# Optimization experiments

Measured on AMD Instinct MI355X. Metric: run time of the kernel, lower is better.

## Reference

```python
import jax, jax.numpy as jnp
import numpy as np

N_NODES = 100000
N_EDGES = 1600000
F_IN, HID, N_CLS = 512, 256, 40


def setup_inputs() -> dict:
    key = jax.random.key(0)
    k1, k2, k3, k4 = jax.random.split(key, 4)
    features = jax.random.normal(k1, (N_NODES, F_IN), dtype=jnp.float32)
    # Glorot-ish scaled weights
    W1 = jax.random.normal(k2, (F_IN, HID), dtype=jnp.float32) * (1.0 / np.sqrt(F_IN))
    b1 = jnp.zeros((HID,), dtype=jnp.float32)
    W2 = jax.random.normal(k3, (HID, N_CLS), dtype=jnp.float32) * (1.0 / np.sqrt(HID))
    b2 = jnp.zeros((N_CLS,), dtype=jnp.float32)
    edge_index = jax.random.randint(k4, (2, N_EDGES), 0, N_NODES, dtype=jnp.int64)
    return {"features": features, "W1": W1, "b1": b1, "W2": W2, "b2": b2,
            "edge_index": edge_index}


def _gcn_conv(x, W, b, src, dst, n_nodes):
    # PyG GCNConv: h = X W; out = D^{-1/2}(A+I)D^{-1/2} h + b
    h = x @ W  # [N, out]
    # degree with self-loops (in-degree on dst + 1)
    deg = jax.ops.segment_sum(jnp.ones_like(dst, dtype=h.dtype), dst,
                              num_segments=n_nodes) + 1.0
    dinv = jax.lax.rsqrt(deg)  # [N]
    norm = dinv[src] * dinv[dst]  # [E]
    # gather-normalize-scatter over edges, plus self-loop term dinv_i^2 * h_i
    agg = jax.ops.segment_sum(h[src] * norm[:, None], dst, num_segments=n_nodes)
    agg = agg + h * (dinv * dinv)[:, None]
    return agg + b


def reference(features, W1, b1, W2, b2, edge_index):
    src, dst = edge_index[0], edge_index[1]
    n = features.shape[0]
    x = jax.nn.relu(_gcn_conv(features, W1, b1, src, dst, n))
    # dropout is identity in eval mode (training=False)
    x = _gcn_conv(x, W2, b2, src, dst, n)
    return jax.nn.log_softmax(x, axis=1), jax.nn.softmax(x, axis=1)
```

## Files before the change

### kernel.cpp

```cpp
#include <hip/hip_runtime.h>
#include <hip/hip_bf16.h>


#define F_IN 512
#define HID  256
#define NCLS 40
#define NPAD 48

typedef __attribute__((ext_vector_type(8))) short bf16x8;
typedef __attribute__((ext_vector_type(4))) float floatx4;

__device__ inline unsigned short f2bf(float v) {
    unsigned u = __float_as_uint(v);
    u += 0x7fffu + ((u >> 16) & 1u);
    return (unsigned short)(u >> 16);
}
__device__ inline float bf2f(unsigned short u) {
    return __uint_as_float(((unsigned)u) << 16);
}

__device__ inline void gload_lds16(const void* g, void* l) {
    __builtin_amdgcn_global_load_lds(
        (const __attribute__((address_space(1))) unsigned int*)g,
        (__attribute__((address_space(3))) unsigned int*)l, 16, 0, 0);
}

__device__ inline bf16x8 pack8(float4 f0, float4 f1) {
    bf16x8 r;
    r[0] = (short)f2bf(f0.x); r[1] = (short)f2bf(f0.y);
    r[2] = (short)f2bf(f0.z); r[3] = (short)f2bf(f0.w);
    r[4] = (short)f2bf(f1.x); r[5] = (short)f2bf(f1.y);
    r[6] = (short)f2bf(f1.z); r[7] = (short)f2bf(f1.w);
    return r;
}

__global__ void detect64_kernel(const int* __restrict__ ei, int* __restrict__ flag) {
    __shared__ int any_nz;
    if (threadIdx.x == 0) any_nz = 0;
    __syncthreads();
    int nz = 0;
    for (int i = threadIdx.x; i < 4096; i += 256) {
        nz |= (ei[2 * i + 1] != 0);
    }
    if (nz) atomicOr(&any_nz, 1);
    __syncthreads();
    if (threadIdx.x == 0) *flag = any_nz ? 0 : 1;
}

__device__ inline int edge_src(const int* ei, long long E, int e, int is64) {
    return is64 ? ei[2LL * e] : ei[e];
}
__device__ inline int edge_dst(const int* ei, long long E, int e, int is64) {
    return is64 ? ei[2LL * (E + e)] : ei[(int)E + e];
}

__global__ void count_kernel(const int* __restrict__ ei, int E,
                             const int* __restrict__ flag, int* __restrict__ cnt) {
    int e = blockIdx.x * 256 + threadIdx.x;
    if (e >= E) return;
    int is64 = *flag;
    int d = edge_dst(ei, E, e, is64);
    atomicAdd(&cnt[d], 1);
}

__global__ __launch_bounds__(256) void scan_block_sums(const int* __restrict__ cnt,
                                                       int* __restrict__ blockSums, int Nn) {
    __shared__ int sdata[256];
    int b = blockIdx.x, t = threadIdx.x;
    int sum = 0;
    int i0 = b * 1024 + t * 4;
    for (int i = 0; i < 4; ++i) {
        int idx = i0 + i;
        if (idx < Nn) sum += cnt[idx];
    }
    sdata[t] = sum;
    __syncthreads();
    for (int s = 128; s > 0; s >>= 1) {
        if (t < s) sdata[t] += sdata[t + s];
        __syncthreads();
    }
    if (t == 0) blockSums[b] = sdata[0];
}

__global__ void scan_sums_kernel(int* __restrict__ blockSums, int nB,
                                 int* __restrict__ rowStart, int Nn) {
    if (threadIdx.x == 0 && blockIdx.x == 0) {
        int run = 0;
        for (int i = 0; i < nB; ++i) { int v = blockSums[i]; blockSums[i] = run; run += v; }
        rowStart[Nn] = run;
    }
}

__global__ __launch_bounds__(256) void scan_final(const int* __restrict__ cnt,
                                                  const int* __restrict__ blockSumsEx,
                                                  int* __restrict__ rowStart,
                                                  int* __restrict__ rowPos, int Nn) {
    __shared__ int sdata[256];
    int b = blockIdx.x, t = threadIdx.x;
    int base = blockSumsEx[b];
    int vals[4];
    int sum = 0;
    int i0 = b * 1024 + t * 4;
    for (int i = 0; i < 4; ++i) {
        int idx = i0 + i;
        vals[i] = (idx < Nn) ? cnt[idx] : 0;
        sum += vals[i];
    }
    sdata[t] = sum;
    __syncthreads();
    for (int off = 1; off < 256; off <<= 1) {
        int y = (t >= off) ? sdata[t - off] : 0;
        __syncthreads();
        sdata[t] += y;
        __syncthreads();
    }
    int run = base + (sdata[t] - sum);
    for (int i = 0; i < 4; ++i) {
        int idx = i0 + i;
        if (idx < Nn) { rowStart[idx] = run; rowPos[idx] = run; }
        run += vals[i];
    }
}

__global__ void dinv_kernel(const int* __restrict__ cnt, float* __restrict__ dinv, int Nn) {
    int i = blockIdx.x * 256 + threadIdx.x;
    if (i < Nn) dinv[i] = rsqrtf((float)cnt[i] + 1.0f);
}

__global__ void fill_kernel(const int* __restrict__ ei, int E, const int* __restrict__ flag,
                            const float* __restrict__ dinv, int* __restrict__ rowPos,
                            int* __restrict__ csrSrc, float* __restrict__ csrNorm) {
    int e = blockIdx.x * 256 + threadIdx.x;
    if (e >= E) return;
    int is64 = *flag;
    int s = edge_src(ei, E, e, is64);
    int d = edge_dst(ei, E, e, is64);
    int p = atomicAdd(&rowPos[d], 1);
    csrSrc[p] = s;
    csrNorm[p] = dinv[s] * dinv[d];
}

__global__ __launch_bounds__(256) void convertW1t_kernel(const float* __restrict__ W1,
                                                         unsigned short* __restrict__ W1t) {
    int id = blockIdx.x * 256 + threadIdx.x;
    int k = id >> 8, n = id & 255;
    W1t[n * 512 + k] = f2bf(W1[id]);
}

__global__ __launch_bounds__(256) void convertW2t_kernel(const float* __restrict__ W2,
                                                         unsigned short* __restrict__ W2t) {
    int id = blockIdx.x * 256 + threadIdx.x;
    if (id >= NPAD * HID) return;
    int n = id / HID, k = id % HID;
    W2t[id] = (n < NCLS) ? f2bf(W2[k * NCLS + n]) : (unsigned short)0;
}

#define BK 64
__global__ __launch_bounds__(256) void gemm1_mfma_kernel(const float* __restrict__ X,
                                                         const unsigned short* __restrict__ W1t,
                                                         unsigned short* __restrict__ h1, int Nn) {
    __shared__ float As[128 * 64];
    __shared__ unsigned short Bs[128 * 64];
    const int tid = threadIdx.x;
    const int bm = blockIdx.x * 128;
    const int bn = blockIdx.y * 128;
    const int lane = tid & 63, w = tid >> 6;
    const int wr = (w & 1) * 64, wc = (w >> 1) * 64;
    const int lrow = lane & 15, lq = lane >> 4;

    int aRow[8], aK[8], bRow[4], bK[4];
#pragma unroll
    for (int i = 0; i < 8; ++i) {
        int c = i * 256 + w * 64 + lane;
        int row = c >> 4, pslot = c & 15;
        aRow[i] = row; aK[i] = (pslot ^ (row & 15)) * 4;
    }
#pragma unroll
    for (int i = 0; i < 4; ++i) {
        int c = i * 256 + w * 64 + lane;
        int row = c >> 3, pslot = c & 7;
        bRow[i] = row; bK[i] = (pslot ^ (row & 7)) * 8;
    }

    floatx4 acc[4][4];
#pragma unroll
    for (int i = 0; i < 4; ++i)
#pragma unroll
        for (int j = 0; j < 4; ++j)
            acc[i][j] = (floatx4){0.f, 0.f, 0.f, 0.f};

    for (int t = 0; t < F_IN / BK; ++t) {
        const int k0 = t * BK;
        __syncthreads();
#pragma unroll
        for (int i = 0; i < 8; ++i) {
            int srow = bm + aRow[i];
            if (srow >= Nn) srow = Nn - 1;
            gload_lds16(&X[(size_t)srow * F_IN + k0 + aK[i]],
                        &As[(i * 256 + w * 64) * 4]);
        }
#pragma unroll
        for (int i = 0; i < 4; ++i)
            gload_lds16(&W1t[(size_t)(bn + bRow[i]) * F_IN + k0 + bK[i]],
                        &Bs[(i * 256 + w * 64) * 8]);
        __syncthreads();

#pragma unroll
        for (int kh = 0; kh < 2; ++kh) {
            bf16x8 av[4], bv[4];
#pragma unroll
            for (int mt = 0; mt < 4; ++mt) {
                int row = wr + mt * 16 + lrow;
                int m = row & 15;
                int s0 = kh * 8 + lq * 2;
                float4 f0 = *(const float4*)&As[row * 64 + ((s0 ^ m) << 2)];
                float4 f1 = *(const float4*)&As[row * 64 + (((s0 + 1) ^ m) << 2)];
                av[mt] = pack8(f0, f1);
            }
#pragma unroll
            for (int nt = 0; nt < 4; ++nt) {
                int row = wc + nt * 16 + lrow;
                int ls = kh * 4 + lq;
                bv[nt] = *(const bf16x8*)&Bs[row * 64 + ((ls ^ (row & 7)) << 3)];
            }
#pragma unroll
            for (int mt = 0; mt < 4; ++mt)
#pragma unroll
                for (int nt = 0; nt < 4; ++nt)
                    acc[mt][nt] = __builtin_amdgcn_mfma_f32_16x16x32_bf16(
                        bv[nt], av[mt], acc[mt][nt], 0, 0, 0);
        }
    }

#pragma unroll
    for (int mt = 0; mt < 4; ++mt) {
        size_t gm = (size_t)(bm + wr + mt * 16 + lrow);
#pragma unroll
        for (int nt = 0; nt < 4; ++nt) {
            int gn = bn + wc + nt * 16 + lq * 4;
            ushort4 o;
            o.x = f2bf(acc[mt][nt][0]); o.y = f2bf(acc[mt][nt][1]);
            o.z = f2bf(acc[mt][nt][2]); o.w = f2bf(acc[mt][nt][3]);
            *(ushort4*)&h1[gm * HID + gn] = o;
        }
    }
}

__global__ __launch_bounds__(256) void agg1_kernel(const unsigned short* __restrict__ h1,
                                                   const int* __restrict__ rowStart,
                                                   const int* __restrict__ csrSrc,
                                                   const float* __restrict__ csrNorm,
                                                   const float* __restrict__ dinv,
                                                   const float* __restrict__ b1,
                                                   unsigned short* __restrict__ x1b, int Nn) {
    int n = blockIdx.x * 4 + (threadIdx.x >> 6);
    int lane = threadIdx.x & 63;
    if (n >= Nn) return;
    const int half = lane >> 5;
    const int col = lane & 31;
    const char* hb = (const char*)h1 + col * 16;

    float acc[8];
#pragma unroll
    for (int j = 0; j < 8; ++j) acc[j] = 0.f;

    int s0 = rowStart[n], s1 = rowStart[n + 1];
    int e = s0;
    for (; e + 7 < s1; e += 8) {
#pragma unroll
        for (int p = 0; p < 4; ++p) {
            int idx = csrSrc[e + 2 * p + half];
            float nrm = csrNorm[e + 2 * p + half];
            bf16x8 v = *(const bf16x8*)(hb + (unsigned)idx * (unsigned)(HID * 2));
#pragma unroll
            for (int j = 0; j < 8; ++j)
                acc[j] += nrm * bf2f((unsigned short)v[j]);
        }
    }
    for (; e + 1 < s1; e += 2) {
        int idx = csrSrc[e + half];
        float nrm = csrNorm[e + half];
        bf16x8 v = *(const bf16x8*)(hb + (unsigned)idx * (unsigned)(HID * 2));
#pragma unroll
        for (int j = 0; j < 8; ++j)
            acc[j] += nrm * bf2f((unsigned short)v[j]);
    }
    if (e < s1) {
        int idx = csrSrc[e];
        float nrm = half ? 0.f : csrNorm[e];
        bf16x8 v = *(const bf16x8*)(hb + (unsigned)idx * (unsigned)(HID * 2));
#pragma unroll
        for (int j = 0; j < 8; ++j)
            acc[j] += nrm * bf2f((unsigned short)v[j]);
    }

#pragma unroll
    for (int j = 0; j < 8; ++j) acc[j] += __shfl_xor(acc[j], 32);

    if (half == 0) {
        float di = dinv[n];
        float self = di * di;
        bf16x8 hv = *(const bf16x8*)(hb + (unsigned)n * (unsigned)(HID * 2));
        float4 bv0 = *(const float4*)(b1 + col * 8);
        float4 bv1 = *(const float4*)(b1 + col * 8 + 4);
        float bb[8] = {bv0.x, bv0.y, bv0.z, bv0.w, bv1.x, bv1.y, bv1.z, bv1.w};
        bf16x8 o;
#pragma unroll
        for (int j = 0; j < 8; ++j)
            o[j] = (short)f2bf(fmaxf(acc[j] + self * bf2f((unsigned short)hv[j]) + bb[j], 0.f));
        *(bf16x8*)((char*)x1b + (size_t)n * (HID * 2) + col * 16) = o;
    }
}

__global__ __launch_bounds__(256) void gemm2_mfma_kernel(const unsigned short* __restrict__ x1b,
                                                         const unsigned short* __restrict__ W2t,
                                                         unsigned short* __restrict__ h2b) {
    const int tid = threadIdx.x;
    const int lane = tid & 63, w = tid >> 6;
    const int base = blockIdx.x * 128 + w * 32;
    const int lrow = lane & 15, lq = lane >> 4;

    floatx4 acc[2][3];
#pragma unroll
    for (int i = 0; i < 2; ++i)
#pragma unroll
        for (int j = 0; j < 3; ++j)
            acc[i][j] = (floatx4){0.f, 0.f, 0.f, 0.f};

#pragma unroll
    for (int k0 = 0; k0 < HID; k0 += 32) {
        bf16x8 a[2], b[3];
#pragma unroll
        for (int mt = 0; mt < 2; ++mt)
            a[mt] = *(const bf16x8*)&x1b[(size_t)(base + mt * 16 + lrow) * HID + k0 + lq * 8];
#pragma unroll
        for (int nt = 0; nt < 3; ++nt)
            b[nt] = *(const bf16x8*)&W2t[(size_t)(nt * 16 + lrow) * HID + k0 + lq * 8];
#pragma unroll
        for (int mt = 0; mt < 2; ++mt)
#pragma unroll
            for (int nt = 0; nt < 3; ++nt)
                acc[mt][nt] = __builtin_amdgcn_mfma_f32_16x16x32_bf16(
                    b[nt], a[mt], acc[mt][nt], 0, 0, 0);
    }
#pragma unroll
    for (int mt = 0; mt < 2; ++mt) {
        size_t gm = (size_t)(base + mt * 16 + lrow);
#pragma unroll
        for (int nt = 0; nt < 3; ++nt) {
            int gn = nt * 16 + lq * 4;
            ushort4 o;
            o.x = f2bf(acc[mt][nt][0]); o.y = f2bf(acc[mt][nt][1]);
            o.z = f2bf(acc[mt][nt][2]); o.w = f2bf(acc[mt][nt][3]);
            *(ushort4*)&h2b[gm * NPAD + gn] = o;
        }
    }
}

__global__ __launch_bounds__(256) void agg2_kernel(const unsigned short* __restrict__ h2b,
                                                   const int* __restrict__ rowStart,
                                                   const int* __restrict__ csrSrc,
                                                   const float* __restrict__ csrNorm,
                                                   const float* __restrict__ dinv,
                                                   const float* __restrict__ b2,
                                                   float* __restrict__ out, int Nn) {
    int n = blockIdx.x * 4 + (threadIdx.x >> 6);
    int lane = threadIdx.x & 63;
    if (n >= Nn) return;
    bool act = lane < NCLS;
    int cl = act ? lane : 0;
    float acc = 0.f;
    int s0 = rowStart[n], s1 = rowStart[n + 1];
    int e = s0;
    for (; e + 3 < s1; e += 4) {
        int iA = csrSrc[e], iB = csrSrc[e + 1], iC = csrSrc[e + 2], iD = csrSrc[e + 3];
        float nA = csrNorm[e], nB = csrNorm[e + 1], nC = csrNorm[e + 2], nD = csrNorm[e + 3];
        float vA = bf2f(h2b[(size_t)iA * NPAD + cl]);
        float vB = bf2f(h2b[(size_t)iB * NPAD + cl]);
        float vC = bf2f(h2b[(size_t)iC * NPAD + cl]);
        float vD = bf2f(h2b[(size_t)iD * NPAD + cl]);
        acc += nA * vA + nB * vB + nC * vC + nD * vD;
    }
    for (; e < s1; ++e) {
        int s = csrSrc[e];
        acc += csrNorm[e] * bf2f(h2b[(size_t)s * NPAD + cl]);
    }
    float di = dinv[n];
    acc += di * di * bf2f(h2b[(size_t)n * NPAD + cl]) + b2[cl];
    float v = act ? acc : -3.4e38f;
#pragma unroll
    for (int off = 32; off > 0; off >>= 1) v = fmaxf(v, __shfl_xor(v, off));
    float ex = act ? expf(acc - v) : 0.f;
    float ssum = ex;
#pragma unroll
    for (int off = 32; off > 0; off >>= 1) ssum += __shfl_xor(ssum, off);
    if (act) {
        float ls = acc - v - logf(ssum);
        out[(size_t)n * NCLS + lane] = ls;
        out[(size_t)Nn * NCLS + (size_t)n * NCLS + lane] = ex / ssum;
    }
}

extern "C" void kernel_launch(void* const* d_in, const int* in_sizes, int n_in,
                              void* d_out, int out_size, void* d_ws, size_t ws_size,
                              hipStream_t stream) {
    const float* features = (const float*)d_in[0];
    const float* W1 = (const float*)d_in[1];
    const float* b1 = (const float*)d_in[2];
    const float* W2 = (const float*)d_in[3];
    const float* b2 = (const float*)d_in[4];
    const int* edge_index = (const int*)d_in[5];

    const int N = in_sizes[0] / F_IN;
    const int E = in_sizes[5] / 2;
    const int Mpad = (N + 127) & ~127;
    float* out = (float*)d_out;

    auto align256 = [](size_t x) { return (x + 255) & ~(size_t)255; };
    char* w = (char*)d_ws;
    int* cnt        = (int*)w;  w += align256((size_t)N * 4);
    int* rowStart   = (int*)w;  w += align256((size_t)(N + 1) * 4);
    int* rowPos     = (int*)w;  w += align256((size_t)N * 4);
    int* blockSums  = (int*)w;  w += align256(1024 * 4);
    int* flag64     = (int*)w;  w += 256;
    int* csrSrc     = (int*)w;  w += align256((size_t)E * 4);
    float* csrNorm  = (float*)w; w += align256((size_t)E * 4);
    float* dinv     = (float*)w; w += align256((size_t)N * 4);
    unsigned short* W1t = (unsigned short*)w; w += align256((size_t)HID * F_IN * 2);
    unsigned short* W2t = (unsigned short*)w; w += align256((size_t)NPAD * HID * 2);
    unsigned short* h1  = (unsigned short*)w; w += align256((size_t)Mpad * HID * 2);
    unsigned short* x1b = (unsigned short*)w; w += align256((size_t)Mpad * HID * 2);
    unsigned short* h2b = (unsigned short*)w; w += align256((size_t)Mpad * NPAD * 2);
    (void)ws_size;

    const int nB = (N + 1023) / 1024;
    const int eBlocks = (E + 255) / 256;
    const int nBlocks = (N + 255) / 256;
    const int waveBlocks = (N + 3) / 4;

    hipMemsetAsync(cnt, 0, (size_t)N * 4, stream);
    detect64_kernel<<<1, 256, 0, stream>>>(edge_index, flag64);
    count_kernel<<<eBlocks, 256, 0, stream>>>(edge_index, E, flag64, cnt);
    scan_block_sums<<<nB, 256, 0, stream>>>(cnt, blockSums, N);
    scan_sums_kernel<<<1, 64, 0, stream>>>(blockSums, nB, rowStart, N);
    dinv_kernel<<<nBlocks, 256, 0, stream>>>(cnt, dinv, N);
    scan_final<<<nB, 256, 0, stream>>>(cnt, blockSums, rowStart, rowPos, N);
    fill_kernel<<<eBlocks, 256, 0, stream>>>(edge_index, E, flag64, dinv, rowPos,
                                             csrSrc, csrNorm);

    convertW1t_kernel<<<(F_IN * HID) / 256, 256, 0, stream>>>(W1, W1t);
    convertW2t_kernel<<<(NPAD * HID + 255) / 256, 256, 0, stream>>>(W2, W2t);

    dim3 g1(Mpad / 128, HID / 128);
    gemm1_mfma_kernel<<<g1, 256, 0, stream>>>(features, W1t, h1, N);
    agg1_kernel<<<waveBlocks, 256, 0, stream>>>(h1, rowStart, csrSrc, csrNorm, dinv,
                                                b1, x1b, N);
    gemm2_mfma_kernel<<<Mpad / 128, 256, 0, stream>>>(x1b, W2t, h2b);
    agg2_kernel<<<waveBlocks, 256, 0, stream>>>(h2b, rowStart, csrSrc, csrNorm, dinv,
                                                b2, out, N);
}
```

Before: 741.3 us.

## Split layer-1 aggregation into column slices with 16-edge lanes per wave

The layer-1 aggregation kernel now splits the 256 hidden columns into 8 slices of 32 handled by separate blocks, grid-striding over nodes. Each wave covers 16 edges in parallel with 4 lanes per edge instead of 2 edges with 32 lanes. The aim is to keep gathered rows in cache per slice and expose more memory-level parallelism for low-degree nodes. In exchange, each gather is only 64 bytes, index and norm loads are repeated for every slice, and a 4-step shuffle reduction is needed per node.

```diff
diff --git a/kernel.cpp b/kernel.cpp
--- a/kernel.cpp
+++ b/kernel.cpp
@@ -246,6 +246,7 @@
     }
 }
 
+#define AGG1_K 3200
 __global__ __launch_bounds__(256) void agg1_kernel(const unsigned short* __restrict__ h1,
                                                    const int* __restrict__ rowStart,
                                                    const int* __restrict__ csrSrc,
@@ -253,62 +254,47 @@
                                                    const float* __restrict__ dinv,
                                                    const float* __restrict__ b1,
                                                    unsigned short* __restrict__ x1b, int Nn) {
-    int n = blockIdx.x * 4 + (threadIdx.x >> 6);
-    int lane = threadIdx.x & 63;
-    if (n >= Nn) return;
-    const int half = lane >> 5;
-    const int col = lane & 31;
-    const char* hb = (const char*)h1 + col * 16;
-
-    float acc[8];
-#pragma unroll
-    for (int j = 0; j < 8; ++j) acc[j] = 0.f;
-
-    int s0 = rowStart[n], s1 = rowStart[n + 1];
-    int e = s0;
-    for (; e + 7 < s1; e += 8) {
-#pragma unroll
-        for (int p = 0; p < 4; ++p) {
-            int idx = csrSrc[e + 2 * p + half];
-            float nrm = csrNorm[e + 2 * p + half];
-            bf16x8 v = *(const bf16x8*)(hb + (unsigned)idx * (unsigned)(HID * 2));
+    const int slice = blockIdx.x & 7;
+    const int bb = blockIdx.x >> 3;
+    const int wid = threadIdx.x >> 6;
+    const int lane = threadIdx.x & 63;
+    const int eg = lane >> 2;
+    const int lc = lane & 3;
+    const char* hb = (const char*)h1 + slice * 64 + lc * 16;
+
+    const int c0 = slice * 32 + lc * 8;
+    float bia[8];
+#pragma unroll
+    for (int j = 0; j < 8; ++j) bia[j] = b1[c0 + j];
+
+    for (int n = bb * 4 + wid; n < Nn; n += AGG1_K * 4) {
+        float acc[8];
+#pragma unroll
+        for (int j = 0; j < 8; ++j) acc[j] = 0.f;
+        int s0 = rowStart[n], s1 = rowStart[n + 1];
+        for (int e = s0; e + eg < s1; e += 16) {
+            int idx = csrSrc[e + eg];
+            float nrm = csrNorm[e + eg];
+            bf16x8 v = *(const bf16x8*)(hb + (size_t)idx * (HID * 2));
 #pragma unroll
             for (int j = 0; j < 8; ++j)
                 acc[j] += nrm * bf2f((unsigned short)v[j]);
         }
-    }
-    for (; e + 1 < s1; e += 2) {
-        int idx = csrSrc[e + half];
-        float nrm = csrNorm[e + half];
-        bf16x8 v = *(const bf16x8*)(hb + (unsigned)idx * (unsigned)(HID * 2));
-#pragma unroll
-        for (int j = 0; j < 8; ++j)
-            acc[j] += nrm * bf2f((unsigned short)v[j]);
-    }
-    if (e < s1) {
-        int idx = csrSrc[e];
-        float nrm = half ? 0.f : csrNorm[e];
-        bf16x8 v = *(const bf16x8*)(hb + (unsigned)idx * (unsigned)(HID * 2));
-#pragma unroll
-        for (int j = 0; j < 8; ++j)
-            acc[j] += nrm * bf2f((unsigned short)v[j]);
-    }
-
-#pragma unroll
-    for (int j = 0; j < 8; ++j) acc[j] += __shfl_xor(acc[j], 32);
-
-    if (half == 0) {
-        float di = dinv[n];
-        float self = di * di;
-        bf16x8 hv = *(const bf16x8*)(hb + (unsigned)n * (unsigned)(HID * 2));
-        float4 bv0 = *(const float4*)(b1 + col * 8);
-        float4 bv1 = *(const float4*)(b1 + col * 8 + 4);
-        float bb[8] = {bv0.x, bv0.y, bv0.z, bv0.w, bv1.x, bv1.y, bv1.z, bv1.w};
-        bf16x8 o;
-#pragma unroll
-        for (int j = 0; j < 8; ++j)
-            o[j] = (short)f2bf(fmaxf(acc[j] + self * bf2f((unsigned short)hv[j]) + bb[j], 0.f));
-        *(bf16x8*)((char*)x1b + (size_t)n * (HID * 2) + col * 16) = o;
+#pragma unroll
+        for (int off = 4; off < 64; off <<= 1)
+#pragma unroll
+            for (int j = 0; j < 8; ++j) acc[j] += __shfl_xor(acc[j], off);
+
+        if (eg == 0) {
+            float di = dinv[n];
+            float self = di * di;
+            bf16x8 hv = *(const bf16x8*)(hb + (size_t)n * (HID * 2));
+            bf16x8 o;
+#pragma unroll
+            for (int j = 0; j < 8; ++j)
+                o[j] = (short)f2bf(fmaxf(acc[j] + self * bf2f((unsigned short)hv[j]) + bia[j], 0.f));
+            *(bf16x8*)((char*)x1b + (size_t)n * (HID * 2) + slice * 64 + lc * 16) = o;
+        }
     }
 }
 
@@ -453,7 +439,7 @@
 
     dim3 g1(Mpad / 128, HID / 128);
     gemm1_mfma_kernel<<<g1, 256, 0, stream>>>(features, W1t, h1, N);
-    agg1_kernel<<<waveBlocks, 256, 0, stream>>>(h1, rowStart, csrSrc, csrNorm, dinv,
+    agg1_kernel<<<8 * AGG1_K, 256, 0, stream>>>(h1, rowStart, csrSrc, csrNorm, dinv,
                                                 b1, x1b, N);
     gemm2_mfma_kernel<<<Mpad / 128, 256, 0, stream>>>(x1b, W2t, h2b);
     agg2_kernel<<<waveBlocks, 256, 0, stream>>>(h2b, rowStart, csrSrc, csrNorm, dinv,
```

Result: slower. 897.2 us (+21.0%).
